# Kernel optimization log

Hardware: AMD Instinct MI355X
Metric: run time of the kernel (lower is better)

Reference implementation:

```python
import jax, jax.numpy as jnp
import numpy as np

B, S, D, H = 128, 512, 512, 4
DH = D // H

def setup_inputs() -> dict:
    key = jax.random.key(0)
    ks = jax.random.split(key, 12)
    s = 1.0 / np.sqrt(D)
    inp = {
        "x": jax.random.normal(ks[0], (B, S, D), dtype=jnp.float32),
        "Wi": jax.random.uniform(ks[1], (D, D), jnp.float32, -s, s),
        "bi": jnp.zeros((D,), jnp.float32),
        "Wq": jax.random.uniform(ks[2], (D, D), jnp.float32, -s, s),
        "bq": jnp.zeros((D,), jnp.float32),
        "Wk": jax.random.uniform(ks[3], (D, D), jnp.float32, -s, s),
        "bk": jnp.zeros((D,), jnp.float32),
        "Wv": jax.random.uniform(ks[4], (D, D), jnp.float32, -s, s),
        "bv": jnp.zeros((D,), jnp.float32),
        "Wo": jax.random.uniform(ks[5], (D, D), jnp.float32, -s, s),
        "bo": jnp.zeros((D,), jnp.float32),
        "data_lens": jax.random.randint(ks[6], (B,), 1, S + 1, dtype=jnp.int32),
    }
    return inp


def _forward(x, Wi, bi, Wq, bq, Wk, bk, Wv, bv, Wo, bo, data_lens):
    # fc_i applied to the whole sequence up front
    xf = x @ Wi + bi                      # [B, S, D]
    h0 = xf[:, 0, :]                      # initial state = fc_i(x)[:, 0]
    scale = 1.0 / jnp.sqrt(jnp.asarray(DH, xf.dtype))

    def step(h, x_t):
        # h: [B, D] previous state (acts as key and value, kv_len == 1)
        # x_t: [B, D] current input (query)
        q = (x_t @ Wq + bq).reshape(B, H, DH)
        k = (h @ Wk + bk).reshape(B, H, DH)
        v = (h @ Wv + bv).reshape(B, H, DH)
        scores = jnp.sum(q * k, axis=-1, keepdims=True) * scale   # [B, H, 1]
        w = jax.nn.softmax(scores, axis=-1)                       # == 1 (single key)
        attn = (w * v).reshape(B, D)
        h_new = attn @ Wo + bo + x_t                              # residual
        return h_new, h_new

    xs = jnp.transpose(xf, (1, 0, 2))     # [S, B, D]
    _, outs = jax.lax.scan(step, h0, xs)  # [S, B, D]
    outputs = jnp.transpose(outs, (1, 0, 2))                      # [B, S, D]

    idx = (data_lens.astype(jnp.int32) - 1)[:, None, None]        # [B,1,1]
    final_state = jnp.take_along_axis(outputs, idx, axis=1)[:, 0, :]
    return outputs, final_state


def reference(x, Wi, bi, Wq, bq, Wk, bk, Wv, bv, Wo, bo, data_lens):
    return _forward(x, Wi, bi, Wq, bq, Wk, bk, Wv, bv, Wo, bo, data_lens)
```

## Files before the change

### kernel.cpp

```cpp
#include <hip/hip_runtime.h>
#include <hip/hip_bf16.h>

typedef __hip_bfloat16 bf16;
typedef __attribute__((ext_vector_type(8))) short short8;
typedef __attribute__((ext_vector_type(4))) float f32x4;

#define S_LEN 512
#define DIM   512
#define BATCH 128
#define ROWS  (BATCH * S_LEN)

__device__ inline unsigned short f2bu(float f){
    bf16 h = __float2bfloat16(f);
    return *reinterpret_cast<unsigned short*>(&h);
}
__device__ inline float ld_in(const void* p, size_t i, int f32){
    return f32 ? ((const float*)p)[i] : __bfloat162float(((const bf16*)p)[i]);
}

typedef __attribute__((address_space(1))) const unsigned int gu32;
typedef __attribute__((address_space(3))) unsigned int lu32;
__device__ __forceinline__ void gld16(const void* g, void* l){
    __builtin_amdgcn_global_load_lds((gu32*)g, (lu32*)l, 16, 0, 0);
}

__device__ __forceinline__ short8 lds_frag(const unsigned short* base, int row, int koff){
    const unsigned off = ((unsigned)(row*128 + koff*2)) ^ (((unsigned)(row & 7)) << 4);
    return *(const short8*)((const char*)base + off);
}

__global__ void detect_dtype(const unsigned int* __restrict__ x, int* __restrict__ flag)
{
    __shared__ int cnt;
    if (threadIdx.x == 0) cnt = 0;
    __syncthreads();
    int loc = 0;
    for (int i = threadIdx.x; i < 8192; i += 256)
        if (((x[i] >> 7) & 0xFFu) == 0xFFu) loc++;
    atomicAdd(&cnt, loc);
    __syncthreads();
    if (threadIdx.x == 0) *flag = (cnt > 0) ? 1 : 0;
}

__global__ void conv_tr(const void* __restrict__ in, bf16* __restrict__ outp,
                        const int* __restrict__ flagp)
{
    const int f32 = *flagp;
    __shared__ unsigned short tile[32][33];
    const int bx = blockIdx.x, by = blockIdx.y;
    const int tx = threadIdx.x, ty = threadIdx.y;
    #pragma unroll
    for (int j = 0; j < 32; j += 8)
        tile[ty + j][tx] = f2bu(ld_in(in, (size_t)(by*32 + ty + j)*DIM + bx*32 + tx, f32));
    __syncthreads();
    #pragma unroll
    for (int j = 0; j < 32; j += 8) {
        unsigned short u = tile[tx][ty + j];
        outp[(size_t)(bx*32 + ty + j)*DIM + by*32 + tx] = *reinterpret_cast<bf16*>(&u);
    }
}

__global__ void conv_cp(const void* __restrict__ in, bf16* __restrict__ outp,
                        const int* __restrict__ flagp)
{
    const int f32 = *flagp;
    const size_t i = (size_t)blockIdx.x*256 + threadIdx.x;
    outp[i] = __float2bfloat16(ld_in(in, i, f32));
}

__global__ void conv_x(const void* __restrict__ X, size_t eoff, bf16* __restrict__ xb,
                       const int* __restrict__ flagp)
{
    const int f32 = *flagp;
    const size_t i = ((size_t)blockIdx.x*256 + threadIdx.x)*8;
    if (f32) {
        const float* p = (const float*)X + eoff + i;
        float4 a = *(const float4*)p;
        float4 b = *(const float4*)(p + 4);
        __align__(16) unsigned short wv[8];
        wv[0]=f2bu(a.x); wv[1]=f2bu(a.y); wv[2]=f2bu(a.z); wv[3]=f2bu(a.w);
        wv[4]=f2bu(b.x); wv[5]=f2bu(b.y); wv[6]=f2bu(b.z); wv[7]=f2bu(b.w);
        *(uint4*)(xb + i) = *(const uint4*)wv;
    } else {
        *(uint4*)(xb + i) = *(const uint4*)((const bf16*)X + eoff + i);
    }
}

__global__ void cvec_kernel(const bf16* __restrict__ WoT, const void* __restrict__ bv,
                            const void* __restrict__ bo, const void* __restrict__ bi,
                            const int* __restrict__ flagp,
                            float* __restrict__ dvec, float* __restrict__ bvec)
{
    const int f32 = *flagp;
    const int n = blockIdx.x * 4 + (threadIdx.x >> 6);
    const int lane = threadIdx.x & 63;
    float acc = 0.f;
    for (int k = lane; k < DIM; k += 64)
        acc += ld_in(bv, k, f32) * __bfloat162float(WoT[(size_t)n*DIM + k]);
    #pragma unroll
    for (int o = 32; o > 0; o >>= 1) acc += __shfl_down(acc, o, 64);
    if (lane == 0) {
        const float dd = acc + ld_in(bo, n, f32);
        dvec[n] = dd;
        bvec[n] = dd + ld_in(bi, n, f32);
    }
}

__global__ void prep_aux(const float* __restrict__ U0, const float* __restrict__ V0,
                         const float* __restrict__ dvec,
                         bf16* __restrict__ A1, bf16* __restrict__ V0b, bf16* __restrict__ Zr)
{
    const int idx = blockIdx.x * 256 + threadIdx.x;
    const int n = idx & 511;
    A1[idx]  = __float2bfloat16(U0[idx] - dvec[n]);
    V0b[idx] = __float2bfloat16(V0[idx]);
    if (idx < 512) Zr[idx] = __float2bfloat16(0.f);
}

#define TILE_PROLOGUE                                                          \
    __shared__ __align__(16) unsigned short As[128][72];                       \
    __shared__ __align__(16) unsigned short Bs[128][72];                       \
    const int tid  = threadIdx.x;                                              \
    const int lane = tid & 63;                                                 \
    const int wave = tid >> 6;                                                 \
    const int wm = (wave & 1) * 64;                                            \
    const int wn = (wave >> 1) * 64;                                           \
    const int cn = lane & 15;                                                  \
    const int quad = lane >> 4;                                                \
    f32x4 acc[4][4];                                                           \
    _Pragma("unroll")                                                          \
    for (int i = 0; i < 4; ++i)                                                \
        _Pragma("unroll")                                                      \
        for (int j = 0; j < 4; ++j) acc[i][j] = (f32x4){0.f,0.f,0.f,0.f};

#define TILE_MFMA                                                              \
        __syncthreads();                                                       \
        _Pragma("unroll")                                                      \
        for (int ks = 0; ks < 64; ks += 32) {                                  \
            short8 af[4], bfr[4];                                              \
            const int koff = ks + quad*8;                                      \
            _Pragma("unroll")                                                  \
            for (int i = 0; i < 4; ++i) af[i]  = *(const short8*)&As[wm + i*16 + cn][koff]; \
            _Pragma("unroll")                                                  \
            for (int j = 0; j < 4; ++j) bfr[j] = *(const short8*)&Bs[wn + j*16 + cn][koff]; \
            _Pragma("unroll")                                                  \
            for (int i = 0; i < 4; ++i)                                        \
                _Pragma("unroll")                                              \
                for (int j = 0; j < 4; ++j)                                    \
                    acc[i][j] = __builtin_amdgcn_mfma_f32_16x16x32_bf16(af[i], bfr[j], acc[i][j], 0, 0, 0); \
        }                                                                      \
        __syncthreads();

#define STAGE_B(Bt, C0)                                                        \
        {                                                                      \
            int r = tid >> 3; const int c = (tid & 7) * 8;                     \
            _Pragma("unroll")                                                  \
            for (int p = 0; p < 4; ++p, r += 32) {                             \
                uint4 v = *(const uint4*)((Bt) + (size_t)((C0) + r)*DIM + k0 + c); \
                *(uint4*)&Bs[r][c] = v;                                        \
            }                                                                  \
        }

#define STAGE_A_IN(SRC, BASE)                                                  \
                if (f32) {                                                     \
                    const float* sp = (const float*)(SRC) + (BASE);            \
                    float4 a = *(const float4*)sp;                             \
                    float4 b = *(const float4*)(sp + 4);                       \
                    __align__(16) unsigned short w[8];                         \
                    w[0]=f2bu(a.x); w[1]=f2bu(a.y); w[2]=f2bu(a.z); w[3]=f2bu(a.w); \
                    w[4]=f2bu(b.x); w[5]=f2bu(b.y); w[6]=f2bu(b.z); w[7]=f2bu(b.w); \
                    *(uint4*)&As[r][c] = *(const uint4*)w;                     \
                } else {                                                       \
                    *(uint4*)&As[r][c] = *(const uint4*)((const bf16*)(SRC) + (BASE)); \
                }

__global__ __launch_bounds__(256) void gemm_sq(const bf16* __restrict__ A,
        const bf16* __restrict__ Btm, bf16* __restrict__ Pout, bf16* __restrict__ Tout)
{
    TILE_PROLOGUE
    const int R0 = blockIdx.y * 128;
    const int C0 = blockIdx.x * 128;
    for (int k0 = 0; k0 < DIM; k0 += 64) {
        {
            int r = tid >> 3; const int c = (tid & 7) * 8;
            #pragma unroll
            for (int p = 0; p < 4; ++p, r += 32)
                *(uint4*)&As[r][c] = *(const uint4*)(A + (size_t)(R0 + r)*DIM + k0 + c);
        }
        STAGE_B(Btm, C0)
        TILE_MFMA
    }
    #pragma unroll
    for (int i = 0; i < 4; ++i) {
        const int rowb = R0 + wm + i*16 + quad*4;
        #pragma unroll
        for (int j = 0; j < 4; ++j) {
            const int cc = C0 + wn + j*16 + cn;
            #pragma unroll
            for (int rr = 0; rr < 4; ++rr) {
                const float v = acc[i][j][rr];
                Pout[(size_t)(rowb + rr)*DIM + cc] = __float2bfloat16(v);
                Tout[(size_t)cc*DIM + rowb + rr]  = __float2bfloat16(v);
            }
        }
    }
}

__global__ __launch_bounds__(256) void gemm_row0(const void* __restrict__ X,
        const bf16* __restrict__ WiT, const float* __restrict__ bvec,
        const int* __restrict__ flagp, float* __restrict__ U0)
{
    const int f32 = *flagp;
    TILE_PROLOGUE
    const int C0 = blockIdx.x * 128;
    for (int k0 = 0; k0 < DIM; k0 += 64) {
        {
            int r = tid >> 3; const int c = (tid & 7) * 8;
            #pragma unroll
            for (int p = 0; p < 4; ++p, r += 32) {
                const size_t base = (size_t)r*S_LEN*DIM + k0 + c;
                STAGE_A_IN(X, base)
            }
        }
        STAGE_B(WiT, C0)
        TILE_MFMA
    }
    #pragma unroll
    for (int i = 0; i < 4; ++i) {
        const int rowb = wm + i*16 + quad*4;
        #pragma unroll
        for (int j = 0; j < 4; ++j) {
            const int cc = C0 + wn + j*16 + cn;
            const float bb = bvec[cc];
            #pragma unroll
            for (int rr = 0; rr < 4; ++rr)
                U0[(size_t)(rowb + rr)*DIM + cc] = acc[i][j][rr] + bb;
        }
    }
}

__global__ __launch_bounds__(256) void gemm_v0(const float* __restrict__ U0,
        const bf16* __restrict__ T0, const float* __restrict__ dvec, float* __restrict__ V0)
{
    TILE_PROLOGUE
    const int C0 = blockIdx.x * 128;
    for (int k0 = 0; k0 < DIM; k0 += 64) {
        {
            int r = tid >> 3; const int c = (tid & 7) * 8;
            #pragma unroll
            for (int p = 0; p < 4; ++p, r += 32) {
                __align__(16) unsigned short w[8];
                #pragma unroll
                for (int q = 0; q < 8; ++q)
                    w[q] = f2bu(U0[(size_t)r*DIM + k0 + c + q] - dvec[k0 + c + q]);
                *(uint4*)&As[r][c] = *(const uint4*)w;
            }
        }
        STAGE_B(T0, C0)
        TILE_MFMA
    }
    #pragma unroll
    for (int i = 0; i < 4; ++i) {
        const int rowb = wm + i*16 + quad*4;
        #pragma unroll
        for (int j = 0; j < 4; ++j) {
            const int cc = C0 + wn + j*16 + cn;
            #pragma unroll
            for (int rr = 0; rr < 4; ++rr) {
                const size_t off = (size_t)(rowb + rr)*DIM + cc;
                V0[off] = acc[i][j][rr] + U0[off];
            }
        }
    }
}

template<int MODE, bool TO_OUT>
__global__ __launch_bounds__(256, 3) void gemm_big(
        const bf16* __restrict__ Abf, const bf16* __restrict__ A1,
        const bf16* __restrict__ V0b, const bf16* __restrict__ Zr,
        const bf16* __restrict__ Bt,  const float* __restrict__ Rf,
        float* __restrict__ Of, bf16* __restrict__ Ob,
        void* __restrict__ Oout, size_t eoff, const int* __restrict__ flagp,
        const int shift)
{
    __shared__ __align__(16) unsigned short As[2][64*64];
    __shared__ __align__(16) unsigned short Bs[2][128*64];
    const int tid  = threadIdx.x;
    const int lane = tid & 63;
    const int w    = tid >> 6;
    const int nb = gridDim.x;
    const int p0 = blockIdx.x;
    const int L  = (p0 & 7) * (nb >> 3) + (p0 >> 3);
    const int bx = L & 3, by = L >> 2;
    const int R0 = by * 64, C0 = bx * 128;
    const int wm = (w & 1) * 32;
    const int wn = (w >> 1) * 64;
    const int cn = lane & 15;
    const int quad = lane >> 4;
    f32x4 acc[2][4];
    #pragma unroll
    for (int i = 0; i < 2; ++i)
        #pragma unroll
        for (int j = 0; j < 4; ++j) acc[i][j] = (f32x4){0.f,0.f,0.f,0.f};

    const int lr  = w*8 + (lane >> 3);
    const int lcb = ((lane & 7) ^ (lane >> 3)) * 8;
    const int ldst = w * 512;
    const bf16* aln[2];
    const bf16* bln[4];
    #pragma unroll
    for (int l = 0; l < 2; ++l) {
        const int grow = R0 + l*32 + lr;
        const bf16* a;
        if (MODE == 2) {
            a = Abf + (size_t)grow*DIM;
        } else if (MODE == 1) {
            const int t = grow & (S_LEN - 1);
            if      (t == 0) a = A1  + (size_t)(grow >> 9)*DIM;
            else if (t == 1) a = V0b + (size_t)(grow >> 9)*DIM;
            else             a = Abf + (size_t)(grow - 1)*DIM;
        } else {
            const int t = grow & (S_LEN - 1);
            a = (t >= shift) ? (Abf + (size_t)(grow - shift)*DIM) : Zr;
        }
        aln[l] = a + lcb;
    }
    #pragma unroll
    for (int l = 0; l < 4; ++l)
        bln[l] = Bt + (size_t)(C0 + l*32 + lr)*DIM + lcb;

#define STAGE(BUF, KN)                                                         \
    {                                                                          \
        gld16(aln[0] + (KN), &As[BUF][0*2048 + ldst]);                         \
        gld16(aln[1] + (KN), &As[BUF][1*2048 + ldst]);                         \
        gld16(bln[0] + (KN), &Bs[BUF][0*2048 + ldst]);                         \
        gld16(bln[1] + (KN), &Bs[BUF][1*2048 + ldst]);                         \
        gld16(bln[2] + (KN), &Bs[BUF][2*2048 + ldst]);                         \
        gld16(bln[3] + (KN), &Bs[BUF][3*2048 + ldst]);                         \
    }

    STAGE(0, 0)
    asm volatile("s_waitcnt vmcnt(0)" ::: "memory");
    __builtin_amdgcn_s_barrier();

    #pragma unroll
    for (int kt = 0; kt < 8; ++kt) {
        const int cur = kt & 1;
        if (kt < 7) STAGE(cur ^ 1, (kt + 1) * 64)
        short8 af[2][2], bfr[4][2];
        #pragma unroll
        for (int i = 0; i < 2; ++i) {
            af[i][0] = lds_frag(&As[cur][0], wm + i*16 + cn,      quad*8);
            af[i][1] = lds_frag(&As[cur][0], wm + i*16 + cn, 32 + quad*8);
        }
        #pragma unroll
        for (int j = 0; j < 4; ++j) {
            bfr[j][0] = lds_frag(&Bs[cur][0], wn + j*16 + cn,      quad*8);
            bfr[j][1] = lds_frag(&Bs[cur][0], wn + j*16 + cn, 32 + quad*8);
        }
        __builtin_amdgcn_s_setprio(1);
        #pragma unroll
        for (int i = 0; i < 2; ++i)
            #pragma unroll
            for (int j = 0; j < 4; ++j) {
                acc[i][j] = __builtin_amdgcn_mfma_f32_16x16x32_bf16(af[i][0], bfr[j][0], acc[i][j], 0, 0, 0);
                acc[i][j] = __builtin_amdgcn_mfma_f32_16x16x32_bf16(af[i][1], bfr[j][1], acc[i][j], 0, 0, 0);
            }
        __builtin_amdgcn_s_setprio(0);
        asm volatile("s_waitcnt vmcnt(0)" ::: "memory");
        __builtin_amdgcn_s_barrier();
    }
#undef STAGE

    const int f32o = TO_OUT ? *flagp : 0;
    #pragma unroll
    for (int i = 0; i < 2; ++i) {
        const int rowb = R0 + wm + i*16 + quad*4;
        #pragma unroll
        for (int j = 0; j < 4; ++j) {
            const int cc = C0 + wn + j*16 + cn;
            #pragma unroll
            for (int rr = 0; rr < 4; ++rr) {
                const size_t off = (size_t)(rowb + rr)*DIM + cc;
                const float res = (MODE == 2) ? Rf[cc] : Rf[off];
                const float v = acc[i][j][rr] + res;
                if (TO_OUT) {
                    if (f32o) ((float*)Oout)[eoff + off] = v;
                    else      ((bf16*)Oout)[eoff + off]  = __float2bfloat16(v);
                } else {
                    Of[off] = v;
                    Ob[off] = __float2bfloat16(v);
                }
            }
        }
    }
}

__global__ void gather_final(void* __restrict__ out, const int* __restrict__ lens,
                             const int* __restrict__ flagp)
{
    const int f32 = *flagp;
    const int idx = blockIdx.x * 256 + threadIdx.x;
    const int b = idx >> 9, n = idx & 511;
    int L = lens[b];
    if (L < 1) L = 1;
    if (L > S_LEN) L = S_LEN;
    const size_t src = ((size_t)b*S_LEN + (L - 1))*DIM + n;
    const size_t dst = (size_t)ROWS*DIM + idx;
    if (f32) ((float*)out)[dst] = ((const float*)out)[src];
    else     ((bf16*)out)[dst]  = ((const bf16*)out)[src];
}

extern "C" void kernel_launch(void* const* d_in, const int* in_sizes, int n_in,
                              void* d_out, int out_size, void* d_ws, size_t ws_size,
                              hipStream_t stream)
{
    const void* X  = d_in[0];
    const void* Wi = d_in[1];
    const void* bi = d_in[2];
    const void* Wv = d_in[7];
    const void* bv = d_in[8];
    const void* Wo = d_in[9];
    const void* bo = d_in[10];
    const int* lens = (const int*)d_in[11];
    char* ws = (char*)d_ws;

    const size_t MATB = (size_t)DIM * DIM * sizeof(bf16);
    bf16* WiT = (bf16*)(ws + 0*MATB);
    bf16* WoT = (bf16*)(ws + 1*MATB);
    bf16* Wvb = (bf16*)(ws + 2*MATB);
    bf16* S2  = (bf16*)(ws + 3*MATB);
    bf16* S3  = (bf16*)(ws + 4*MATB);
    bf16* T0  = (bf16*)(ws + 5*MATB);
    bf16* T1  = (bf16*)(ws + 6*MATB);
    bf16* T2  = (bf16*)(ws + 7*MATB);
    bf16* T3  = (bf16*)(ws + 8*MATB);
    size_t off = 9*MATB;
    float* dvec = (float*)(ws + off); off += 2048;
    float* bvec = (float*)(ws + off); off += 2048;
    int*   flag = (int*)  (ws + off); off += 256;
    float* U0   = (float*)(ws + off); off += (size_t)BATCH*DIM*4;
    float* V0   = (float*)(ws + off); off += (size_t)BATCH*DIM*4;
    bf16*  A1   = (bf16*) (ws + off); off += (size_t)BATCH*DIM*2;
    bf16*  V0b  = (bf16*) (ws + off); off += (size_t)BATCH*DIM*2;
    bf16*  Zr   = (bf16*) (ws + off); off += 1024;
    off = (off + 1023) & ~(size_t)1023;
    char* dyn = ws + off;
    const size_t avail = ws_size > off ? ws_size - off : 0;

    int CR = 512;
    for (long cr = 65536; cr >= 512; cr >>= 1)
        if ((size_t)cr * 7168 <= avail) { CR = (int)cr; break; }

    bf16*  xbf = (bf16*) dyn;
    float* Uf  = (float*)(dyn + (size_t)CR*1024);
    bf16*  Ub  = (bf16*) (dyn + (size_t)CR*3072);
    float* Vf  = (float*)(dyn + (size_t)CR*4096);
    bf16*  Vb  = (bf16*) (dyn + (size_t)CR*6144);

    detect_dtype<<<1, 256, 0, stream>>>((const unsigned int*)X, flag);
    conv_tr<<<dim3(16,16), dim3(32,8), 0, stream>>>(Wi, WiT, flag);
    conv_tr<<<dim3(16,16), dim3(32,8), 0, stream>>>(Wo, WoT, flag);
    conv_cp<<<1024, 256, 0, stream>>>(Wv, Wvb, flag);
    cvec_kernel<<<128, 256, 0, stream>>>(WoT, bv, bo, bi, flag, dvec, bvec);
    gemm_sq<<<dim3(4,4), 256, 0, stream>>>(Wvb, WoT, S2, T0);
    gemm_sq<<<dim3(4,4), 256, 0, stream>>>(S2, T0, S3, T1);
    gemm_sq<<<dim3(4,4), 256, 0, stream>>>(S3, T1, S2, T2);
    gemm_sq<<<dim3(4,4), 256, 0, stream>>>(S2, T2, S3, T3);
    gemm_row0<<<dim3(4,1), 256, 0, stream>>>(X, WiT, bvec, flag, U0);
    gemm_v0<<<dim3(4,1), 256, 0, stream>>>(U0, T0, dvec, V0);
    prep_aux<<<256, 256, 0, stream>>>(U0, V0, dvec, A1, V0b, Zr);

    const int NC = ROWS / CR;
    const int nb = (CR / 64) * 4;
    for (int c = 0; c < NC; ++c) {
        const size_t eoff = (size_t)c*CR*DIM;
        const size_t boff = (size_t)(c*(CR/S_LEN))*DIM;
        conv_x<<<CR/4, 256, 0, stream>>>(X, eoff, xbf, flag);
        gemm_big<2,false><<<nb, 256, 0, stream>>>(xbf, nullptr, nullptr, Zr,
                WiT, bvec, Uf, Ub, nullptr, 0, flag, 0);
        gemm_big<1,false><<<nb, 256, 0, stream>>>(Ub, A1 + boff, V0b + boff, Zr,
                T0, Uf, Vf, Vb, nullptr, 0, flag, 1);
        gemm_big<0,false><<<nb, 256, 0, stream>>>(Vb, nullptr, nullptr, Zr,
                T1, Vf, Uf, Ub, nullptr, 0, flag, 2);
        gemm_big<0,false><<<nb, 256, 0, stream>>>(Ub, nullptr, nullptr, Zr,
                T2, Uf, Vf, Vb, nullptr, 0, flag, 4);
        gemm_big<0,true ><<<nb, 256, 0, stream>>>(Vb, nullptr, nullptr, Zr,
                T3, Vf, nullptr, nullptr, d_out, eoff, flag, 8);
    }
    gather_final<<<256, 256, 0, stream>>>(d_out, lens, flag);
}
```

Measured before the change: 963.7 us.

## Triple-buffer LDS tiles in gemm_big with partial vmcnt waits

Changes the big GEMM k-loop from double to triple buffering. Two tiles are prefetched ahead, and each step waits only for the oldest batch of loads using vmcnt counts. The aim is to hide global-to-LDS load latency behind MFMA work instead of draining all loads every iteration. In exchange, LDS use per block grows to about 72KB and the launch bound drops from 3 to 2 blocks per CU, which lowers occupancy.

```diff
diff --git a/kernel.cpp b/kernel.cpp
--- a/kernel.cpp
+++ b/kernel.cpp
@@ -275,7 +275,7 @@
 }
 
 template<int MODE, bool TO_OUT>
-__global__ __launch_bounds__(256, 3) void gemm_big(
+__global__ __launch_bounds__(256, 2) void gemm_big(
         const bf16* __restrict__ Abf, const bf16* __restrict__ A1,
         const bf16* __restrict__ V0b, const bf16* __restrict__ Zr,
         const bf16* __restrict__ Bt,  const float* __restrict__ Rf,
@@ -283,8 +283,8 @@
         void* __restrict__ Oout, size_t eoff, const int* __restrict__ flagp,
         const int shift)
 {
-    __shared__ __align__(16) unsigned short As[2][64*64];
-    __shared__ __align__(16) unsigned short Bs[2][128*64];
+    __shared__ __align__(16) unsigned short As[3][64*64];
+    __shared__ __align__(16) unsigned short Bs[3][128*64];
     const int tid  = threadIdx.x;
     const int lane = tid & 63;
     const int w    = tid >> 6;
@@ -329,47 +329,57 @@
     for (int l = 0; l < 4; ++l)
         bln[l] = Bt + (size_t)(C0 + l*32 + lr)*DIM + lcb;
 
-#define STAGE(BUF, KN)                                                         \
+#define STAGE(SLOT, KN)                                                        \
     {                                                                          \
-        gld16(aln[0] + (KN), &As[BUF][0*2048 + ldst]);                         \
-        gld16(aln[1] + (KN), &As[BUF][1*2048 + ldst]);                         \
-        gld16(bln[0] + (KN), &Bs[BUF][0*2048 + ldst]);                         \
-        gld16(bln[1] + (KN), &Bs[BUF][1*2048 + ldst]);                         \
-        gld16(bln[2] + (KN), &Bs[BUF][2*2048 + ldst]);                         \
-        gld16(bln[3] + (KN), &Bs[BUF][3*2048 + ldst]);                         \
+        gld16(aln[0] + (KN), &As[SLOT][0*2048 + ldst]);                        \
+        gld16(aln[1] + (KN), &As[SLOT][1*2048 + ldst]);                        \
+        gld16(bln[0] + (KN), &Bs[SLOT][0*2048 + ldst]);                        \
+        gld16(bln[1] + (KN), &Bs[SLOT][1*2048 + ldst]);                        \
+        gld16(bln[2] + (KN), &Bs[SLOT][2*2048 + ldst]);                        \
+        gld16(bln[3] + (KN), &Bs[SLOT][3*2048 + ldst]);                        \
     }
 
     STAGE(0, 0)
-    asm volatile("s_waitcnt vmcnt(0)" ::: "memory");
-    __builtin_amdgcn_s_barrier();
-
-    #pragma unroll
-    for (int kt = 0; kt < 8; ++kt) {
-        const int cur = kt & 1;
-        if (kt < 7) STAGE(cur ^ 1, (kt + 1) * 64)
-        short8 af[2][2], bfr[4][2];
-        #pragma unroll
-        for (int i = 0; i < 2; ++i) {
-            af[i][0] = lds_frag(&As[cur][0], wm + i*16 + cn,      quad*8);
-            af[i][1] = lds_frag(&As[cur][0], wm + i*16 + cn, 32 + quad*8);
-        }
-        #pragma unroll
-        for (int j = 0; j < 4; ++j) {
-            bfr[j][0] = lds_frag(&Bs[cur][0], wn + j*16 + cn,      quad*8);
-            bfr[j][1] = lds_frag(&Bs[cur][0], wn + j*16 + cn, 32 + quad*8);
-        }
-        __builtin_amdgcn_s_setprio(1);
-        #pragma unroll
-        for (int i = 0; i < 2; ++i)
-            #pragma unroll
-            for (int j = 0; j < 4; ++j) {
-                acc[i][j] = __builtin_amdgcn_mfma_f32_16x16x32_bf16(af[i][0], bfr[j][0], acc[i][j], 0, 0, 0);
-                acc[i][j] = __builtin_amdgcn_mfma_f32_16x16x32_bf16(af[i][1], bfr[j][1], acc[i][j], 0, 0, 0);
-            }
-        __builtin_amdgcn_s_setprio(0);
-        asm volatile("s_waitcnt vmcnt(0)" ::: "memory");
-        __builtin_amdgcn_s_barrier();
-    }
+    STAGE(1, 64)
+    STAGE(2, 128)
+
+#define STEP(U, VM)                                                            \
+    {                                                                          \
+        asm volatile("s_waitcnt vmcnt(" #VM ")" ::: "memory");                 \
+        __builtin_amdgcn_s_barrier();                                          \
+        const unsigned short* Ac = &As[(U) % 3][0];                            \
+        const unsigned short* Bc = &Bs[(U) % 3][0];                            \
+        short8 af[2][2], bfr[4][2];                                            \
+        _Pragma("unroll")                                                      \
+        for (int i = 0; i < 2; ++i) {                                          \
+            af[i][0] = lds_frag(Ac, wm + i*16 + cn,      quad*8);              \
+            af[i][1] = lds_frag(Ac, wm + i*16 + cn, 32 + quad*8);              \
+        }                                                                      \
+        _Pragma("unroll")                                                      \
+        for (int j = 0; j < 4; ++j) {                                          \
+            bfr[j][0] = lds_frag(Bc, wn + j*16 + cn,      quad*8);             \
+            bfr[j][1] = lds_frag(Bc, wn + j*16 + cn, 32 + quad*8);             \
+        }                                                                      \
+        _Pragma("unroll")                                                      \
+        for (int i = 0; i < 2; ++i)                                            \
+            _Pragma("unroll")                                                  \
+            for (int j = 0; j < 4; ++j) {                                      \
+                acc[i][j] = __builtin_amdgcn_mfma_f32_16x16x32_bf16(af[i][0], bfr[j][0], acc[i][j], 0, 0, 0); \
+                acc[i][j] = __builtin_amdgcn_mfma_f32_16x16x32_bf16(af[i][1], bfr[j][1], acc[i][j], 0, 0, 0); \
+            }                                                                  \
+        __builtin_amdgcn_s_barrier();                                          \
+        if ((U) + 3 < 8) STAGE((U) % 3, ((U) + 3) * 64)                        \
+    }
+
+    STEP(0, 12)
+    STEP(1, 12)
+    STEP(2, 12)
+    STEP(3, 12)
+    STEP(4, 12)
+    STEP(5, 12)
+    STEP(6, 6)
+    STEP(7, 0)
+#undef STEP
 #undef STAGE
 
     const int f32o = TO_OUT ? *flagp : 0;
```

After: 1.023 ms. +6.1%, slower.
